# Kernel tuning notes

Measured on AMD Instinct MI355X. Metric: run time of the kernel, lower is better.

## Reference

```python
import jax, jax.numpy as jnp
import numpy as np

N_EMBD = 1024
N_HEAD = 16
B, T, T_MEM = 4, 1024, 1024


def setup_inputs() -> dict:
    key = jax.random.key(0)
    ks = jax.random.split(key, 11)
    s = 1.0 / np.sqrt(N_EMBD)
    return {
        "q_in": jax.random.normal(ks[0], (B, T, N_EMBD), jnp.float32),
        "k_in": jax.random.normal(ks[1], (B, T_MEM, N_EMBD), jnp.float32),
        "v_in": jax.random.normal(ks[2], (B, T_MEM, N_EMBD), jnp.float32),
        # torch nn.Linear weights: [out_features, in_features]
        "Wq": jax.random.normal(ks[3], (N_EMBD, N_EMBD), jnp.float32) * s,
        "bq": jax.random.normal(ks[4], (N_EMBD,), jnp.float32) * s,
        "Wk": jax.random.normal(ks[5], (N_EMBD, N_EMBD), jnp.float32) * s,
        "bk": jax.random.normal(ks[6], (N_EMBD,), jnp.float32) * s,
        "Wv": jax.random.normal(ks[7], (N_EMBD, N_EMBD), jnp.float32) * s,
        "bv": jax.random.normal(ks[8], (N_EMBD,), jnp.float32) * s,
        "Wo": jax.random.normal(ks[9], (N_EMBD, N_EMBD), jnp.float32) * s,
        "bo": jax.random.normal(ks[10], (N_EMBD,), jnp.float32) * s,
    }


def reference(q_in, k_in, v_in, Wq, bq, Wk, bk, Wv, bv, Wo, bo):
    b, t, c = q_in.shape
    t_mem = k_in.shape[1]
    hd = c // N_HEAD  # head dim

    def proj(x, W, bias):
        return x @ W.T + bias

    # [b, h, t, hd]
    q = proj(q_in, Wq, bq).reshape(b, t, N_HEAD, hd).transpose(0, 2, 1, 3)
    k = proj(k_in, Wk, bk).reshape(b, t_mem, N_HEAD, hd).transpose(0, 2, 1, 3)
    v = proj(v_in, Wv, bv).reshape(b, t_mem, N_HEAD, hd).transpose(0, 2, 1, 3)

    scale = 1.0 / np.sqrt(hd).astype(np.float32)
    att = jnp.einsum("bhqd,bhkd->bhqk", q, k) * scale
    att = jax.nn.softmax(att, axis=-1)  # dropout p=0 -> identity

    y = jnp.einsum("bhqk,bhkd->bhqd", att, v)
    y = y.transpose(0, 2, 1, 3).reshape(b, t, c)
    y = proj(y, Wo, bo)  # resid_drop p=0 -> identity

    attention = jnp.mean(att, axis=1)  # mean over heads: [b, t, t_mem]
    return (y, attention)
```

## Files before the change

kernel.cpp:

```cpp
#include <hip/hip_runtime.h>
#include <hip/hip_fp16.h>


typedef __attribute__((ext_vector_type(8))) short s16x8;
typedef __attribute__((ext_vector_type(4))) float f32x4;
typedef __attribute__((ext_vector_type(4))) unsigned short u16x4;

#define N_EMBD 1024
#define NH 16
#define BT 4096
#define STR 1032

#if __has_builtin(__builtin_amdgcn_global_load_lds)
#define HAVE_GLL 1
#define GLDS16(g, l)                                                              \
  __builtin_amdgcn_global_load_lds((__attribute__((address_space(1))) void*)(g), \
                                   (__attribute__((address_space(3))) void*)(l), 16, 0, 0)
#else
#define HAVE_GLL 0
#endif

static __device__ __forceinline__ unsigned short f2bf(float f) {
  unsigned int u = __builtin_bit_cast(unsigned int, f);
  u += 0x7FFFu + ((u >> 16) & 1u);
  return (unsigned short)(u >> 16);
}
static __device__ __forceinline__ float bf2f(unsigned short h) {
  return __builtin_bit_cast(float, ((unsigned int)h) << 16);
}

__global__ __launch_bounds__(256) void cvt_in3(const float* __restrict__ q,
                                               const float* __restrict__ k,
                                               const float* __restrict__ v,
                                               unsigned short* __restrict__ out) {
  const int z = blockIdx.z;
  const float* src = (z == 0) ? q : (z == 1 ? k : v);
  int i = (blockIdx.x * 256 + threadIdx.x) * 4;
  float4 val = *(const float4*)(src + i);
  u16x4 o;
  o[0] = f2bf(val.x);
  o[1] = f2bf(val.y);
  o[2] = f2bf(val.z);
  o[3] = f2bf(val.w);
  *(u16x4*)(out + (size_t)z * BT * N_EMBD + i) = o;
}

__global__ __launch_bounds__(256) void cvt_w4(const float* __restrict__ wo,
                                              const float* __restrict__ wq,
                                              const float* __restrict__ wk,
                                              const float* __restrict__ wv,
                                              unsigned short* __restrict__ out) {
  const int z = blockIdx.z;
  const float* src = (z == 0) ? wo : (z == 1 ? wq : (z == 2 ? wk : wv));
  const float scale = (z == 1) ? 0.125f : 1.0f;
  int i = (blockIdx.x * 256 + threadIdx.x) * 4;
  float4 val = *(const float4*)(src + i);
  u16x4 o;
  o[0] = f2bf(val.x * scale);
  o[1] = f2bf(val.y * scale);
  o[2] = f2bf(val.z * scale);
  o[3] = f2bf(val.w * scale);
  *(u16x4*)(out + (size_t)z * N_EMBD * N_EMBD + i) = o;
}

template <bool F32OUT>
static __device__ __forceinline__ void gemm_bt_tile(const unsigned short* __restrict__ A,
                                                    const unsigned short* __restrict__ B,
                                                    const float* __restrict__ bias, float bscale,
                                                    void* __restrict__ Cout,
                                                    int m0, int n0, int N, int K,
                                                    unsigned short* Al, unsigned short* Bl) {
  const int tid = threadIdx.x;
  const int l = tid & 63, w = tid >> 6;
  const int wr = w >> 1, wc = w & 1;
  const int l15 = l & 15, l4 = l >> 4;
  const int srow = tid >> 3;
  const int skk = (tid & 7) * 8;
  f32x4 acc[4][4] = {};
  for (int k0 = 0; k0 < K; k0 += 64) {
#if HAVE_GLL
#pragma unroll
    for (int i = 0; i < 4; ++i) {
      GLDS16(&A[(size_t)(m0 + i * 32 + srow) * K + k0 + skk], Al + i * 2048 + w * 512);
      GLDS16(&B[(size_t)(n0 + i * 32 + srow) * K + k0 + skk], Bl + i * 2048 + w * 512);
    }
#else
#pragma unroll
    for (int i = 0; i < 4; ++i) {
      int row = i * 32 + srow;
      *(s16x8*)&Al[row * 64 + skk] = *(const s16x8*)&A[(size_t)(m0 + row) * K + k0 + skk];
      *(s16x8*)&Bl[row * 64 + skk] = *(const s16x8*)&B[(size_t)(n0 + row) * K + k0 + skk];
    }
#endif
    __syncthreads();
#pragma unroll
    for (int kf = 0; kf < 2; ++kf) {
      s16x8 af[4], bfr[4];
#pragma unroll
      for (int mi = 0; mi < 4; ++mi)
        af[mi] = *(const s16x8*)&Al[(wr * 64 + mi * 16 + l15) * 64 + kf * 32 + l4 * 8];
#pragma unroll
      for (int nj = 0; nj < 4; ++nj)
        bfr[nj] = *(const s16x8*)&Bl[(wc * 64 + nj * 16 + l15) * 64 + kf * 32 + l4 * 8];
#pragma unroll
      for (int mi = 0; mi < 4; ++mi) {
#pragma unroll
        for (int nj = 0; nj < 4; ++nj)
          acc[mi][nj] =
              __builtin_amdgcn_mfma_f32_16x16x32_bf16(af[mi], bfr[nj], acc[mi][nj], 0, 0, 0);
      }
    }
    __syncthreads();
  }
#pragma unroll
  for (int nj = 0; nj < 4; ++nj) {
    int col = n0 + wc * 64 + nj * 16 + l15;
    float bv = bias[col] * bscale;
#pragma unroll
    for (int mi = 0; mi < 4; ++mi) {
#pragma unroll
      for (int r = 0; r < 4; ++r) {
        int row = m0 + wr * 64 + mi * 16 + l4 * 4 + r;
        float v = acc[mi][nj][r] + bv;
        if constexpr (F32OUT)
          ((float*)Cout)[(size_t)row * N + col] = v;
        else
          ((unsigned short*)Cout)[(size_t)row * N + col] = f2bf(v);
      }
    }
  }
}

__global__ __launch_bounds__(256) void gemm_qkv(const unsigned short* __restrict__ Xin,
                                                const unsigned short* __restrict__ Wbf,
                                                const float* __restrict__ bq,
                                                const float* __restrict__ bk,
                                                const float* __restrict__ bv,
                                                unsigned short* __restrict__ Cout) {
  __shared__ unsigned short Al[128 * 64];
  __shared__ unsigned short Bl[128 * 64];
  const int z = blockIdx.z;
  const float* bias = (z == 0) ? bq : (z == 1 ? bk : bv);
  const float bscale = (z == 0) ? 0.125f : 1.0f;
  gemm_bt_tile<false>(Xin + (size_t)z * BT * N_EMBD,
                      Wbf + (size_t)(1 + z) * N_EMBD * N_EMBD, bias, bscale,
                      Cout + (size_t)z * BT * N_EMBD, blockIdx.x * 128, blockIdx.y * 128,
                      N_EMBD, N_EMBD, Al, Bl);
}

__global__ __launch_bounds__(256) void gemm_out(const unsigned short* __restrict__ Ybf,
                                                const unsigned short* __restrict__ Wo,
                                                const float* __restrict__ bo,
                                                float* __restrict__ Cout) {
  __shared__ unsigned short Al[128 * 64];
  __shared__ unsigned short Bl[128 * 64];
  gemm_bt_tile<true>(Ybf, Wo, bo, 1.0f, Cout, blockIdx.x * 128, blockIdx.y * 128, N_EMBD, N_EMBD,
                     Al, Bl);
}

__global__ __launch_bounds__(256) void transpose_v(const unsigned short* __restrict__ Vp,
                                                   unsigned short* __restrict__ Vt) {
  __shared__ unsigned short tile[64][65];
  const int t0 = blockIdx.x * 64, h = blockIdx.y, b = blockIdx.z;
  const int r = threadIdx.x >> 2, c0 = (threadIdx.x & 3) * 16;
  const unsigned short* src = Vp + (size_t)(b * 1024 + t0 + r) * 1024 + h * 64 + c0;
#pragma unroll
  for (int j = 0; j < 16; ++j) tile[r][c0 + j] = src[j];
  __syncthreads();
  unsigned short* dst = Vt + (size_t)((b * 16 + h) * 64 + r) * 1024 + t0 + c0;
#pragma unroll
  for (int j = 0; j < 16; ++j) dst[j] = tile[c0 + j][r];
}

__global__ __launch_bounds__(1024, 4) void attn_ph2(const unsigned short* __restrict__ Qp,
                                                    const unsigned short* __restrict__ Kp,
                                                    const unsigned short* __restrict__ Vt,
                                                    unsigned short* __restrict__ Ybf,
                                                    unsigned short* __restrict__ Pmean) {
  __shared__ __align__(16) unsigned short S2[2][32 * STR];
  __shared__ float RedM[2][32][8];
  __shared__ float RedS[2][32][4];
  const int tid = threadIdx.x;
  const int tm = tid >> 9;
  const int ttid = tid & 511;
  const int w4 = ttid >> 6;
  const int l = tid & 63;
  const int l15 = l & 15, l4 = l >> 4;
  const int qg = w4 & 1;
  const int gnr = w4 >> 1;
  const int qgw = w4 >> 2;
  const int dtw = w4 & 3;

  const int bid = blockIdx.x;
  const int grp = bid & 7, qt = bid >> 3;
  const int b = grp >> 1, hg = grp & 1;
  const int q0 = qt * 32;

  __half2 am[32];
#pragma unroll
  for (int j = 0; j < 32; ++j) am[j] = __float2half2_rn(0.f);

#pragma unroll 1
  for (int it = 0; it < 4; ++it) {
    const int h = hg * 8 + it * 2 + tm;
    const unsigned short* qbase =
        Qp + (size_t)(b * 1024 + q0 + qg * 16 + l15) * 1024 + h * 64 + l4 * 8;
    s16x8 aq0 = *(const s16x8*)qbase;
    s16x8 aq1 = *(const s16x8*)(qbase + 32);
    f32x4 sacc[16];
    float m = -3.4e38f;
    __builtin_amdgcn_s_setprio(1);
#pragma unroll
    for (int nt = 0; nt < 16; ++nt) {
      int gn = gnr * 16 + nt;
      const unsigned short* kb = Kp + (size_t)(b * 1024 + gn * 16 + l15) * 1024 + h * 64 + l4 * 8;
      f32x4 s = {};
      s = __builtin_amdgcn_mfma_f32_16x16x32_bf16(*(const s16x8*)kb, aq0, s, 0, 0, 0);
      s = __builtin_amdgcn_mfma_f32_16x16x32_bf16(*(const s16x8*)(kb + 32), aq1, s, 0, 0, 0);
      sacc[nt] = s;
#pragma unroll
      for (int rr = 0; rr < 4; ++rr) m = fmaxf(m, s[rr]);
    }
    __builtin_amdgcn_s_setprio(0);
    m = fmaxf(m, __shfl_xor(m, 16));
    m = fmaxf(m, __shfl_xor(m, 32));
    if (l < 16) RedM[tm][qg * 16 + l][w4] = m;
    __syncthreads();

    const int row = qg * 16 + l15;
    float mm = RedM[tm][row][0];
#pragma unroll
    for (int j = 1; j < 8; ++j) mm = fmaxf(mm, RedM[tm][row][j]);
    float ps = 0.f;
#pragma unroll
    for (int nt = 0; nt < 16; ++nt) {
      float e0 = __expf(sacc[nt][0] - mm);
      float e1 = __expf(sacc[nt][1] - mm);
      float e2 = __expf(sacc[nt][2] - mm);
      float e3 = __expf(sacc[nt][3] - mm);
      ps += (e0 + e1) + (e2 + e3);
      unsigned int lo, hi;
      asm("v_cvt_pk_bf16_f32 %0, %1, %2" : "=v"(lo) : "v"(e0), "v"(e1));
      asm("v_cvt_pk_bf16_f32 %0, %1, %2" : "=v"(hi) : "v"(e2), "v"(e3));
      uint2 pk;
      pk.x = lo;
      pk.y = hi;
      *(uint2*)&S2[tm][row * STR + (gnr * 16 + nt) * 16 + l4 * 4] = pk;
    }
    ps += __shfl_xor(ps, 16);
    ps += __shfl_xor(ps, 32);
    if (l < 16) RedS[tm][qg * 16 + l][gnr] = ps;
    __syncthreads();

    float lsA = RedS[tm][qgw * 16 + l15][0] + RedS[tm][qgw * 16 + l15][1] +
                RedS[tm][qgw * 16 + l15][2] + RedS[tm][qgw * 16 + l15][3];
    float fac = 0.0625f / lsA;
    f32x4 y = {};
    const unsigned short* vb =
        Vt + (size_t)((b * 16 + h) * 64 + dtw * 16 + l15) * 1024 + l4 * 8;
    __builtin_amdgcn_s_setprio(1);
#pragma unroll
    for (int kq = 0; kq < 4; ++kq) {
#pragma unroll
      for (int kk = 0; kk < 8; ++kk) {
        const int ks = kq * 8 + kk;
        s16x8 pa = *(const s16x8*)&S2[tm][(qgw * 16 + l15) * STR + ks * 32 + l4 * 8];
        y = __builtin_amdgcn_mfma_f32_16x16x32_bf16(pa, *(const s16x8*)(vb + ks * 32), y, 0, 0, 0);
        if (kq == dtw) {
#pragma unroll
          for (int e2 = 0; e2 < 4; ++e2) {
            float2 fv;
            fv.x = bf2f((unsigned short)pa[e2 * 2]) * fac;
            fv.y = bf2f((unsigned short)pa[e2 * 2 + 1]) * fac;
            am[kk * 4 + e2] = __hadd2(am[kk * 4 + e2], __float22half2_rn(fv));
          }
        }
      }
    }
    __builtin_amdgcn_s_setprio(0);
#pragma unroll
    for (int rr = 0; rr < 4; ++rr) {
      int row2 = qgw * 16 + l4 * 4 + rr;
      float lsr = RedS[tm][row2][0] + RedS[tm][row2][1] + RedS[tm][row2][2] + RedS[tm][row2][3];
      Ybf[(size_t)(b * 1024 + q0 + row2) * 1024 + h * 64 + dtw * 16 + l15] = f2bf(y[rr] / lsr);
    }
    __syncthreads();
  }

  unsigned int* us = (unsigned int*)S2;
  if (tm == 1) {
#pragma unroll
    for (int j = 0; j < 32; ++j) us[ttid * 32 + j] = __builtin_bit_cast(unsigned int, am[j]);
  }
  __syncthreads();
  if (tm == 0) {
    unsigned short* pm = Pmean + ((size_t)(b * 2 + hg) << 20) +
                         (size_t)(q0 + qgw * 16 + l15) * 1024 + dtw * 256 + l4 * 8;
#pragma unroll
    for (int kk = 0; kk < 8; ++kk) {
      s16x8 ov;
#pragma unroll
      for (int e2 = 0; e2 < 4; ++e2) {
        int j = kk * 4 + e2;
        __half2 ot = __builtin_bit_cast(__half2, us[ttid * 32 + j]);
        float2 fo = __half22float2(ot);
        float2 fm = __half22float2(am[j]);
        ov[e2 * 2] = (short)f2bf(fm.x + fo.x);
        ov[e2 * 2 + 1] = (short)f2bf(fm.y + fo.y);
      }
      *(s16x8*)&pm[kk * 32] = ov;
    }
  }
}

__global__ __launch_bounds__(256) void mean2(const unsigned short* __restrict__ P2,
                                             float* __restrict__ out) {
  size_t f = ((size_t)blockIdx.x * 256 + threadIdx.x) * 8;
  int b = (int)(f >> 20);
  size_t i0 = f + ((size_t)b << 20);
  s16x8 a = *(const s16x8*)&P2[i0];
  s16x8 d = *(const s16x8*)&P2[i0 + (1u << 20)];
  float4 o0, o1;
  o0.x = bf2f((unsigned short)a[0]) + bf2f((unsigned short)d[0]);
  o0.y = bf2f((unsigned short)a[1]) + bf2f((unsigned short)d[1]);
  o0.z = bf2f((unsigned short)a[2]) + bf2f((unsigned short)d[2]);
  o0.w = bf2f((unsigned short)a[3]) + bf2f((unsigned short)d[3]);
  o1.x = bf2f((unsigned short)a[4]) + bf2f((unsigned short)d[4]);
  o1.y = bf2f((unsigned short)a[5]) + bf2f((unsigned short)d[5]);
  o1.z = bf2f((unsigned short)a[6]) + bf2f((unsigned short)d[6]);
  o1.w = bf2f((unsigned short)a[7]) + bf2f((unsigned short)d[7]);
  *(float4*)&out[f] = o0;
  *(float4*)&out[f + 4] = o1;
}

extern "C" void kernel_launch(void* const* d_in, const int* in_sizes, int n_in, void* d_out,
                              int out_size, void* d_ws, size_t ws_size, hipStream_t stream) {
  const float* q_in = (const float*)d_in[0];
  const float* k_in = (const float*)d_in[1];
  const float* v_in = (const float*)d_in[2];
  const float* Wq = (const float*)d_in[3];
  const float* bq = (const float*)d_in[4];
  const float* Wk = (const float*)d_in[5];
  const float* bk = (const float*)d_in[6];
  const float* Wv = (const float*)d_in[7];
  const float* bv = (const float*)d_in[8];
  const float* Wo = (const float*)d_in[9];
  const float* bo = (const float*)d_in[10];

  float* out_y = (float*)d_out;
  float* out_att = out_y + (size_t)BT * N_EMBD;

  char* ws = (char*)d_ws;
  const size_t MB = 1024 * 1024;
  unsigned short* xin_bf = (unsigned short*)(ws);
  unsigned short* W_bf = (unsigned short*)(ws + 24 * MB);
  unsigned short* Qp = (unsigned short*)(ws + 32 * MB);
  unsigned short* Kp = Qp + (size_t)BT * N_EMBD;
  unsigned short* Vp = Kp + (size_t)BT * N_EMBD;
  unsigned short* Pmean = (unsigned short*)(ws);
  unsigned short* Vt = (unsigned short*)(ws + 16 * MB);
  unsigned short* Ybf = Vp;

  const int NIN = BT * N_EMBD;
  const int NW = N_EMBD * N_EMBD;

  cvt_in3<<<dim3(NIN / 1024, 1, 3), 256, 0, stream>>>(q_in, k_in, v_in, xin_bf);
  cvt_w4<<<dim3(NW / 1024, 1, 4), 256, 0, stream>>>(Wo, Wq, Wk, Wv, W_bf);

  gemm_qkv<<<dim3(BT / 128, N_EMBD / 128, 3), 256, 0, stream>>>(xin_bf, W_bf, bq, bk, bv, Qp);
  transpose_v<<<dim3(16, 16, 4), 256, 0, stream>>>(Vp, Vt);
  attn_ph2<<<256, 1024, 0, stream>>>(Qp, Kp, Vt, Ybf, Pmean);
  mean2<<<2048, 256, 0, stream>>>(Pmean, out_att);
  gemm_out<<<dim3(BT / 128, N_EMBD / 128), 256, 0, stream>>>(Ybf, W_bf, bo, out_y);
}
```

Measured before the change: 244.8 us.

## Restructure attention kernel to 16-query tiles with split-K PV and LDS reduction

Replaces the 32-query, two-heads-in-parallel attention kernel with a 16-query-per-block variant that processes one head at a time and launches twice as many blocks. Raw scores are stored to LDS as bf16, then each thread re-reads a 16-element row slice to compute exp and the row sum. The PV product is split over four K quarters and reduced through an LDS buffer. The aim is more blocks for better CU occupancy and smaller register footprint (no 16-tile score array, smaller mean accumulator). In exchange it adds an extra score round-trip through LDS, bf16 rounding of the scores before the exp (a precision loss), and an extra reduction sync per head.

Measured after the change: 242.6 us. Within noise of the previous version (-0.9%).

```diff
diff --git a/kernel.cpp b/kernel.cpp
--- a/kernel.cpp
+++ b/kernel.cpp
@@ -27,6 +27,11 @@
 }
 static __device__ __forceinline__ float bf2f(unsigned short h) {
   return __builtin_bit_cast(float, ((unsigned int)h) << 16);
+}
+static __device__ __forceinline__ unsigned int pk_bf16(float lo, float hi) {
+  unsigned int r;
+  asm("v_cvt_pk_bf16_f32 %0, %1, %2" : "=v"(r) : "v"(lo), "v"(hi));
+  return r;
 }
 
 __global__ __launch_bounds__(256) void cvt_in3(const float* __restrict__ q,
@@ -172,141 +177,150 @@
   for (int j = 0; j < 16; ++j) dst[j] = tile[c0 + j][r];
 }
 
-__global__ __launch_bounds__(1024, 4) void attn_ph2(const unsigned short* __restrict__ Qp,
+__global__ __launch_bounds__(1024, 4) void attn_q16(const unsigned short* __restrict__ Qp,
                                                     const unsigned short* __restrict__ Kp,
                                                     const unsigned short* __restrict__ Vt,
                                                     unsigned short* __restrict__ Ybf,
                                                     unsigned short* __restrict__ Pmean) {
-  __shared__ __align__(16) unsigned short S2[2][32 * STR];
-  __shared__ float RedM[2][32][8];
-  __shared__ float RedS[2][32][4];
+  __shared__ __align__(16) unsigned short S2[16 * STR];
+  __shared__ float RedM[16][16];
+  __shared__ float RedS[16][16];
+  __shared__ float Yred[4][16][66];
   const int tid = threadIdx.x;
-  const int tm = tid >> 9;
-  const int ttid = tid & 511;
-  const int w4 = ttid >> 6;
-  const int l = tid & 63;
+  const int w = tid >> 6, l = tid & 63;
   const int l15 = l & 15, l4 = l >> 4;
-  const int qg = w4 & 1;
-  const int gnr = w4 >> 1;
-  const int qgw = w4 >> 2;
-  const int dtw = w4 & 3;
+  const int r = tid & 15, c = tid >> 4;
+  const int dtw = w & 3, kqw = w >> 2;
 
   const int bid = blockIdx.x;
   const int grp = bid & 7, qt = bid >> 3;
   const int b = grp >> 1, hg = grp & 1;
-  const int q0 = qt * 32;
-
-  __half2 am[32];
-#pragma unroll
-  for (int j = 0; j < 32; ++j) am[j] = __float2half2_rn(0.f);
+  const int q0 = qt * 16;
+
+  __half2 am[8];
+#pragma unroll
+  for (int j = 0; j < 8; ++j) am[j] = __float2half2_rn(0.f);
 
 #pragma unroll 1
-  for (int it = 0; it < 4; ++it) {
-    const int h = hg * 8 + it * 2 + tm;
-    const unsigned short* qbase =
-        Qp + (size_t)(b * 1024 + q0 + qg * 16 + l15) * 1024 + h * 64 + l4 * 8;
+  for (int it = 0; it < 8; ++it) {
+    const int h = hg * 8 + it;
+    const unsigned short* qbase = Qp + (size_t)(b * 1024 + q0 + l15) * 1024 + h * 64 + l4 * 8;
     s16x8 aq0 = *(const s16x8*)qbase;
     s16x8 aq1 = *(const s16x8*)(qbase + 32);
-    f32x4 sacc[16];
     float m = -3.4e38f;
     __builtin_amdgcn_s_setprio(1);
 #pragma unroll
-    for (int nt = 0; nt < 16; ++nt) {
-      int gn = gnr * 16 + nt;
+    for (int nt = 0; nt < 4; ++nt) {
+      const int gn = w * 4 + nt;
       const unsigned short* kb = Kp + (size_t)(b * 1024 + gn * 16 + l15) * 1024 + h * 64 + l4 * 8;
       f32x4 s = {};
       s = __builtin_amdgcn_mfma_f32_16x16x32_bf16(*(const s16x8*)kb, aq0, s, 0, 0, 0);
       s = __builtin_amdgcn_mfma_f32_16x16x32_bf16(*(const s16x8*)(kb + 32), aq1, s, 0, 0, 0);
-      sacc[nt] = s;
-#pragma unroll
-      for (int rr = 0; rr < 4; ++rr) m = fmaxf(m, s[rr]);
+      u16x4 p;
+#pragma unroll
+      for (int rr = 0; rr < 4; ++rr) {
+        m = fmaxf(m, s[rr]);
+        p[rr] = f2bf(s[rr]);
+      }
+      *(u16x4*)&S2[l15 * STR + gn * 16 + l4 * 4] = p;
     }
     __builtin_amdgcn_s_setprio(0);
     m = fmaxf(m, __shfl_xor(m, 16));
     m = fmaxf(m, __shfl_xor(m, 32));
-    if (l < 16) RedM[tm][qg * 16 + l][w4] = m;
-    __syncthreads();
-
-    const int row = qg * 16 + l15;
-    float mm = RedM[tm][row][0];
-#pragma unroll
-    for (int j = 1; j < 8; ++j) mm = fmaxf(mm, RedM[tm][row][j]);
-    float ps = 0.f;
-#pragma unroll
-    for (int nt = 0; nt < 16; ++nt) {
-      float e0 = __expf(sacc[nt][0] - mm);
-      float e1 = __expf(sacc[nt][1] - mm);
-      float e2 = __expf(sacc[nt][2] - mm);
-      float e3 = __expf(sacc[nt][3] - mm);
-      ps += (e0 + e1) + (e2 + e3);
-      unsigned int lo, hi;
-      asm("v_cvt_pk_bf16_f32 %0, %1, %2" : "=v"(lo) : "v"(e0), "v"(e1));
-      asm("v_cvt_pk_bf16_f32 %0, %1, %2" : "=v"(hi) : "v"(e2), "v"(e3));
-      uint2 pk;
-      pk.x = lo;
-      pk.y = hi;
-      *(uint2*)&S2[tm][row * STR + (gnr * 16 + nt) * 16 + l4 * 4] = pk;
-    }
+    if (l < 16) RedM[w][l] = m;
+    __syncthreads();
+
+    float mm = RedM[0][r];
+#pragma unroll
+    for (int j = 1; j < 16; ++j) mm = fmaxf(mm, RedM[j][r]);
+    unsigned short* sp = &S2[r * STR + c * 16];
+    s16x8 sv0 = *(const s16x8*)sp;
+    s16x8 sv1 = *(const s16x8*)(sp + 8);
+    float e0 = __expf(bf2f((unsigned short)sv0[0]) - mm);
+    float e1 = __expf(bf2f((unsigned short)sv0[1]) - mm);
+    float e2 = __expf(bf2f((unsigned short)sv0[2]) - mm);
+    float e3 = __expf(bf2f((unsigned short)sv0[3]) - mm);
+    float e4 = __expf(bf2f((unsigned short)sv0[4]) - mm);
+    float e5 = __expf(bf2f((unsigned short)sv0[5]) - mm);
+    float e6 = __expf(bf2f((unsigned short)sv0[6]) - mm);
+    float e7 = __expf(bf2f((unsigned short)sv0[7]) - mm);
+    float f0 = __expf(bf2f((unsigned short)sv1[0]) - mm);
+    float f1 = __expf(bf2f((unsigned short)sv1[1]) - mm);
+    float f2 = __expf(bf2f((unsigned short)sv1[2]) - mm);
+    float f3 = __expf(bf2f((unsigned short)sv1[3]) - mm);
+    float f4 = __expf(bf2f((unsigned short)sv1[4]) - mm);
+    float f5 = __expf(bf2f((unsigned short)sv1[5]) - mm);
+    float f6 = __expf(bf2f((unsigned short)sv1[6]) - mm);
+    float f7 = __expf(bf2f((unsigned short)sv1[7]) - mm);
+    float ps = (((e0 + e1) + (e2 + e3)) + ((e4 + e5) + (e6 + e7))) +
+               (((f0 + f1) + (f2 + f3)) + ((f4 + f5) + (f6 + f7)));
+    uint4 pv0, pv1;
+    pv0.x = pk_bf16(e0, e1);
+    pv0.y = pk_bf16(e2, e3);
+    pv0.z = pk_bf16(e4, e5);
+    pv0.w = pk_bf16(e6, e7);
+    pv1.x = pk_bf16(f0, f1);
+    pv1.y = pk_bf16(f2, f3);
+    pv1.z = pk_bf16(f4, f5);
+    pv1.w = pk_bf16(f6, f7);
+    *(uint4*)sp = pv0;
+    *(uint4*)(sp + 8) = pv1;
     ps += __shfl_xor(ps, 16);
     ps += __shfl_xor(ps, 32);
-    if (l < 16) RedS[tm][qg * 16 + l][gnr] = ps;
-    __syncthreads();
-
-    float lsA = RedS[tm][qgw * 16 + l15][0] + RedS[tm][qgw * 16 + l15][1] +
-                RedS[tm][qgw * 16 + l15][2] + RedS[tm][qgw * 16 + l15][3];
-    float fac = 0.0625f / lsA;
+    if (l < 16) RedS[w][l] = ps;
+    __syncthreads();
+
+    float Lq = RedS[0][l15];
+#pragma unroll
+    for (int j = 1; j < 16; ++j) Lq += RedS[j][l15];
+    const float fac = 0.0625f / Lq;
     f32x4 y = {};
     const unsigned short* vb =
         Vt + (size_t)((b * 16 + h) * 64 + dtw * 16 + l15) * 1024 + l4 * 8;
     __builtin_amdgcn_s_setprio(1);
 #pragma unroll
-    for (int kq = 0; kq < 4; ++kq) {
-#pragma unroll
-      for (int kk = 0; kk < 8; ++kk) {
-        const int ks = kq * 8 + kk;
-        s16x8 pa = *(const s16x8*)&S2[tm][(qgw * 16 + l15) * STR + ks * 32 + l4 * 8];
-        y = __builtin_amdgcn_mfma_f32_16x16x32_bf16(pa, *(const s16x8*)(vb + ks * 32), y, 0, 0, 0);
-        if (kq == dtw) {
-#pragma unroll
-          for (int e2 = 0; e2 < 4; ++e2) {
-            float2 fv;
-            fv.x = bf2f((unsigned short)pa[e2 * 2]) * fac;
-            fv.y = bf2f((unsigned short)pa[e2 * 2 + 1]) * fac;
-            am[kk * 4 + e2] = __hadd2(am[kk * 4 + e2], __float22half2_rn(fv));
-          }
+    for (int kk = 0; kk < 8; ++kk) {
+      const int ks = kqw * 8 + kk;
+      s16x8 pa = *(const s16x8*)&S2[l15 * STR + ks * 32 + l4 * 8];
+      y = __builtin_amdgcn_mfma_f32_16x16x32_bf16(pa, *(const s16x8*)(vb + ks * 32), y, 0, 0, 0);
+      if ((kk >> 1) == dtw) {
+#pragma unroll
+        for (int e2i = 0; e2i < 4; ++e2i) {
+          float2 fv;
+          fv.x = bf2f((unsigned short)pa[e2i * 2]) * fac;
+          fv.y = bf2f((unsigned short)pa[e2i * 2 + 1]) * fac;
+          am[(kk & 1) * 4 + e2i] = __hadd2(am[(kk & 1) * 4 + e2i], __float22half2_rn(fv));
         }
       }
     }
     __builtin_amdgcn_s_setprio(0);
 #pragma unroll
-    for (int rr = 0; rr < 4; ++rr) {
-      int row2 = qgw * 16 + l4 * 4 + rr;
-      float lsr = RedS[tm][row2][0] + RedS[tm][row2][1] + RedS[tm][row2][2] + RedS[tm][row2][3];
-      Ybf[(size_t)(b * 1024 + q0 + row2) * 1024 + h * 64 + dtw * 16 + l15] = f2bf(y[rr] / lsr);
-    }
-    __syncthreads();
+    for (int rr = 0; rr < 4; ++rr) Yred[kqw][l4 * 4 + rr][dtw * 16 + l15] = y[rr];
+    __syncthreads();
+
+    {
+      const int erow = w;
+      const int ed = tid & 63;
+      float s4 = ((Yred[0][erow][ed] + Yred[1][erow][ed]) +
+                  (Yred[2][erow][ed] + Yred[3][erow][ed]));
+      float Lr = RedS[0][erow];
+#pragma unroll
+      for (int j = 1; j < 16; ++j) Lr += RedS[j][erow];
+      Ybf[(size_t)(b * 1024 + q0 + erow) * 1024 + h * 64 + ed] = f2bf(s4 / Lr);
+    }
   }
 
-  unsigned int* us = (unsigned int*)S2;
-  if (tm == 1) {
-#pragma unroll
-    for (int j = 0; j < 32; ++j) us[ttid * 32 + j] = __builtin_bit_cast(unsigned int, am[j]);
-  }
-  __syncthreads();
-  if (tm == 0) {
-    unsigned short* pm = Pmean + ((size_t)(b * 2 + hg) << 20) +
-                         (size_t)(q0 + qgw * 16 + l15) * 1024 + dtw * 256 + l4 * 8;
-#pragma unroll
-    for (int kk = 0; kk < 8; ++kk) {
+  {
+    unsigned short* pm =
+        Pmean + ((size_t)(b * 2 + hg) << 20) + (size_t)(q0 + l15) * 1024 + w * 64 + l4 * 8;
+#pragma unroll
+    for (int kk = 0; kk < 2; ++kk) {
       s16x8 ov;
 #pragma unroll
-      for (int e2 = 0; e2 < 4; ++e2) {
-        int j = kk * 4 + e2;
-        __half2 ot = __builtin_bit_cast(__half2, us[ttid * 32 + j]);
-        float2 fo = __half22float2(ot);
-        float2 fm = __half22float2(am[j]);
-        ov[e2 * 2] = (short)f2bf(fm.x + fo.x);
-        ov[e2 * 2 + 1] = (short)f2bf(fm.y + fo.y);
+      for (int e2i = 0; e2i < 4; ++e2i) {
+        float2 fm = __half22float2(am[kk * 4 + e2i]);
+        ov[e2i * 2] = (short)f2bf(fm.x);
+        ov[e2i * 2 + 1] = (short)f2bf(fm.y);
       }
       *(s16x8*)&pm[kk * 32] = ov;
     }
@@ -369,7 +383,7 @@
 
   gemm_qkv<<<dim3(BT / 128, N_EMBD / 128, 3), 256, 0, stream>>>(xin_bf, W_bf, bq, bk, bv, Qp);
   transpose_v<<<dim3(16, 16, 4), 256, 0, stream>>>(Vp, Vt);
-  attn_ph2<<<256, 1024, 0, stream>>>(Qp, Kp, Vt, Ybf, Pmean);
+  attn_q16<<<512, 1024, 0, stream>>>(Qp, Kp, Vt, Ybf, Pmean);
   mean2<<<2048, 256, 0, stream>>>(Pmean, out_att);
   gemm_out<<<dim3(BT / 128, N_EMBD / 128), 256, 0, stream>>>(Ybf, W_bf, bo, out_y);
 }
```
